# Optimization experiments

Measured on AMD Instinct MI355X. Metric: run time of the kernel, lower is better.

Reference implementation:

```python
import jax, jax.numpy as jnp
import numpy as np

T, S, N, E, H, FF = 1024, 2048, 4, 1024, 16, 4096
HD = E // H
EPS = 1e-5


def layer_norm(x, g, b):
    mu = jnp.mean(x, axis=-1, keepdims=True)
    var = jnp.mean(jnp.square(x - mu), axis=-1, keepdims=True)
    return (x - mu) / jnp.sqrt(var + EPS) * g + b


def mha(q_in, k_in, v_in, w_in, b_in, w_out, b_out):
    # q_in: (T,N,E), k_in/v_in: (S,N,E); matches torch F.linear with (3E,E) weight
    t, n, e = q_in.shape
    s = k_in.shape[0]
    wq, wk, wv = jnp.split(w_in, 3, axis=0)
    bq, bk, bv = jnp.split(b_in, 3)
    q = (q_in @ wq.T + bq) * (HD ** -0.5)
    k = k_in @ wk.T + bk
    v = v_in @ wv.T + bv
    # (L,N,E) -> (N*H, L, HD)
    q = q.reshape(t, n * H, HD).transpose(1, 0, 2)
    k = k.reshape(s, n * H, HD).transpose(1, 0, 2)
    v = v.reshape(s, n * H, HD).transpose(1, 0, 2)
    attn = jax.nn.softmax(jnp.einsum('bth,bsh->bts', q, k), axis=-1)
    out = jnp.einsum('bts,bsh->bth', attn, v)  # (N*H, T, HD)
    out = out.transpose(1, 0, 2).reshape(t, n, e)
    return out @ w_out.T + b_out


def setup_inputs() -> dict:
    key = jax.random.key(0)
    ks = jax.random.split(key, 16)
    p = lambda k, shape: jax.random.normal(k, shape, dtype=jnp.float32) * 0.02
    return {
        'tgt': jax.random.normal(ks[0], (T, N, E), dtype=jnp.float32),
        'memory': jax.random.normal(ks[1], (S, N, E), dtype=jnp.float32),
        'sa_w_in': p(ks[2], (3 * E, E)), 'sa_b_in': jnp.zeros((3 * E,), jnp.float32),
        'sa_w_out': p(ks[3], (E, E)), 'sa_b_out': jnp.zeros((E,), jnp.float32),
        'ca_w_in': p(ks[4], (3 * E, E)), 'ca_b_in': jnp.zeros((3 * E,), jnp.float32),
        'ca_w_out': p(ks[5], (E, E)), 'ca_b_out': jnp.zeros((E,), jnp.float32),
        'w1': p(ks[6], (FF, E)), 'b1': jnp.zeros((FF,), jnp.float32),
        'w2': p(ks[7], (E, FF)), 'b2': jnp.zeros((E,), jnp.float32),
        'ln1_g': jnp.ones((E,), jnp.float32), 'ln1_b': jnp.zeros((E,), jnp.float32),
        'ln2_g': jnp.ones((E,), jnp.float32), 'ln2_b': jnp.zeros((E,), jnp.float32),
        'ln3_g': jnp.ones((E,), jnp.float32), 'ln3_b': jnp.zeros((E,), jnp.float32),
    }


def reference(tgt, memory, sa_w_in, sa_b_in, sa_w_out, sa_b_out,
              ca_w_in, ca_b_in, ca_w_out, ca_b_out,
              w1, b1, w2, b2, ln1_g, ln1_b, ln2_g, ln2_b, ln3_g, ln3_b):
    # self-attention block (post-LN residual); dropout = identity (eval mode)
    tgt2 = mha(tgt, tgt, tgt, sa_w_in, sa_b_in, sa_w_out, sa_b_out)
    x = layer_norm(tgt + tgt2, ln1_g, ln1_b)
    # cross-attention block
    tgt2 = mha(x, memory, memory, ca_w_in, ca_b_in, ca_w_out, ca_b_out)
    x = layer_norm(x + tgt2, ln2_g, ln2_b)
    # FFN with relu
    tgt2 = jax.nn.relu(x @ w1.T + b1) @ w2.T + b2
    return layer_norm(x + tgt2, ln3_g, ln3_b)
```

## Files before the change

### kernel.cpp

```cpp
#include <hip/hip_runtime.h>


typedef __bf16 bf16x8 __attribute__((ext_vector_type(8)));
typedef float  f32x4  __attribute__((ext_vector_type(4)));
typedef float  f32x16 __attribute__((ext_vector_type(16)));

#define T_  1024
#define S_  2048
#define NB_ 4
#define E_  1024
#define H_  16
#define HD_ 64
#define FF_ 4096
#define M1_ (T_*NB_)
#define M2_ (S_*NB_)
#define LOG2E 1.44269504088896f

__device__ __forceinline__ unsigned short f2bf(float f){
  unsigned int u = __builtin_bit_cast(unsigned int, f);
  u += 0x7fffu + ((u>>16)&1u);
  return (unsigned short)(u>>16);
}
__device__ __forceinline__ float bf2f(unsigned short h){
  unsigned int u = ((unsigned int)h)<<16;
  return __builtin_bit_cast(float, u);
}

__device__ __forceinline__ void gload16(unsigned short* l, const unsigned short* g){
  __builtin_amdgcn_global_load_lds(
      (const __attribute__((address_space(1))) unsigned int*)g,
      (__attribute__((address_space(3))) unsigned int*)l, 16, 0, 0);
}

__device__ __forceinline__ void perm32swap(unsigned &a, unsigned &b){
  asm("v_permlane32_swap_b32 %0, %1" : "+v"(a), "+v"(b));
}

__device__ __forceinline__ int loff(int row, int kc){
  return ((row>>1)<<6) + (((((row&1)<<2)|kc) ^ ((row>>1)&7))<<3);
}

struct CvtSeg { const float* s; unsigned short* d; int n4; };
struct CvtArgs { CvtSeg seg[8]; int blk_end[8]; };
__global__ __launch_bounds__(256) void f2b_multi_k(CvtArgs a){
  const int b = blockIdx.x;
  int si = 0;
  #pragma unroll
  for (int i=0;i<8;i++) if (b >= a.blk_end[i]) si = i+1;
  const int base = si ? a.blk_end[si-1] : 0;
  const int i4 = (b - base)*256 + threadIdx.x;
  if (i4 >= a.seg[si].n4) return;
  float4 f = ((const float4*)a.seg[si].s)[i4];
  union { unsigned short u[4]; uint2 v; } t;
  t.u[0]=f2bf(f.x); t.u[1]=f2bf(f.y); t.u[2]=f2bf(f.z); t.u[3]=f2bf(f.w);
  ((uint2*)a.seg[si].d)[i4] = t.v;
}

template<int FLAGS>
__global__ __launch_bounds__(512, 2) void gemm8_k(
    const unsigned short* __restrict__ A, int lda,
    const unsigned short* __restrict__ B, int ldb,
    const float* __restrict__ bias,
    unsigned short* __restrict__ Cb,
    int M, int N, int K)
{
  __shared__ unsigned short a_sh[4][256*32];
  __shared__ unsigned short b_sh[4][256*32];
  const int tid  = threadIdx.x;
  const int wave = tid>>6, lane = tid&63;
  const int l15 = lane&15, l4 = lane>>4;

  int bid = blockIdx.x;
  if ((gridDim.x & 7) == 0){ const int cpx = gridDim.x>>3; bid = (bid&7)*cpx + (bid>>3); }
  const int nbm = M>>8;
  const int bm = bid % nbm, bn = bid / nbm;
  const int brow = bm<<8, bcol = bn<<8;
  const int wm0 = (wave>>2)*128, wn = (wave&3)*64;
  const int NT = K>>5;

  int ldsl[2]; const unsigned short* pA[2]; const unsigned short* pB[2];
  #pragma unroll
  for (int i=0;i<2;i++){
    const int l = i*512 + wave*64 + lane;
    const int grp = l>>3, sl = (l&7) ^ (grp&7);
    const int row = (grp<<1)|(sl>>2), c = sl&3;
    ldsl[i] = l<<3;
    pA[i] = A + (size_t)(brow + row)*lda + (c<<3);
    pB[i] = B + (size_t)(bcol + row)*ldb + (c<<3);
  }

  f32x4 acc[8][4] = {};

  auto stageA = [&](int t){
    unsigned short* s = a_sh[t&3];
    #pragma unroll
    for (int i=0;i<2;i++) gload16(&s[ldsl[i]], pA[i] + t*32);
  };
  auto stageB = [&](int t){
    unsigned short* s = b_sh[t&3];
    #pragma unroll
    for (int i=0;i<2;i++) gload16(&s[ldsl[i]], pB[i] + t*32);
  };

  stageA(0); stageB(0); stageA(1); stageB(1);
  asm volatile("s_waitcnt vmcnt(4)" ::: "memory");
  __builtin_amdgcn_s_barrier();

  for (int t=0; t<NT; ++t){
    const unsigned short* as = a_sh[t&3];
    const unsigned short* bs = b_sh[t&3];
    const bool pre = (t+2 < NT);

    if (pre) stageA(t+2);
    bf16x8 bf[4], af[4];
    #pragma unroll
    for (int n=0;n<4;n++) bf[n] = *(const bf16x8*)&bs[loff(wn + n*16 + l15, l4)];
    #pragma unroll
    for (int m=0;m<4;m++) af[m] = *(const bf16x8*)&as[loff(wm0 + m*16 + l15, l4)];
    __builtin_amdgcn_s_setprio(1);
    #pragma unroll
    for (int m=0;m<4;m++)
      #pragma unroll
      for (int n=0;n<4;n++)
        acc[m][n] = __builtin_amdgcn_mfma_f32_16x16x32_bf16(af[m], bf[n], acc[m][n], 0,0,0);
    __builtin_amdgcn_s_setprio(0);
    __builtin_amdgcn_s_barrier();

    if (pre) stageB(t+2);
    #pragma unroll
    for (int m=0;m<4;m++) af[m] = *(const bf16x8*)&as[loff(wm0 + 64 + m*16 + l15, l4)];
    __builtin_amdgcn_s_setprio(1);
    #pragma unroll
    for (int m=0;m<4;m++)
      #pragma unroll
      for (int n=0;n<4;n++)
        acc[4+m][n] = __builtin_amdgcn_mfma_f32_16x16x32_bf16(af[m], bf[n], acc[4+m][n], 0,0,0);
    __builtin_amdgcn_s_setprio(0);
    if (pre) asm volatile("s_waitcnt vmcnt(4)" ::: "memory");
    else     asm volatile("s_waitcnt vmcnt(0)" ::: "memory");
    __builtin_amdgcn_s_barrier();
  }

  #pragma unroll
  for (int mi=0;mi<8;mi++){
    #pragma unroll
    for (int r=0;r<4;r++){
      const int rr = brow + wm0 + mi*16 + l4*4 + r;
      #pragma unroll
      for (int n=0;n<4;n++){
        const int cc = bcol + wn + n*16 + l15;
        float v = acc[mi][n][r] + bias[cc];
        if (FLAGS & 1) v = fmaxf(v, 0.f);
        Cb[(size_t)rr*N + cc] = f2bf(v);
      }
    }
  }
}

template<int FLAGS, int BN>
__global__ __launch_bounds__(256) void gemm_k(
    const unsigned short* __restrict__ A, int lda,
    const unsigned short* __restrict__ B, int ldb,
    const float* __restrict__ bias,
    const float* __restrict__ res,
    unsigned short* __restrict__ Cb, float* __restrict__ Cf,
    int M, int N, int K)
{
  constexpr int NW = BN/32;
  __shared__ unsigned short a_sh[128*64];
  __shared__ unsigned short b_sh[BN*64];
  const int tid  = threadIdx.x;
  const int wave = tid>>6;
  const int lane = tid&63;
  const int l15 = lane&15, l4 = lane>>4;
  const int row0 = blockIdx.x*128, col0 = blockIdx.y*BN;
  const int wm = (wave>>1)*64, wn = (wave&1)*(BN/2);

  const int lrow = tid>>3;
  const int scol = ((tid&7) ^ (lrow&7)) << 3;
  const int dst8 = (tid&7) << 3;

  f32x4 acc[4][NW] = {};

  for (int k0=0; k0<K; k0+=64){
    const unsigned short* ga = A + (size_t)(row0+lrow)*lda + k0 + scol;
    const unsigned short* gb = B + (size_t)(col0+lrow)*ldb + k0 + scol;
    #pragma unroll
    for (int i=0;i<4;i++)
      gload16(&a_sh[(lrow + i*32)*64 + dst8], ga + (size_t)(i*32)*lda);
    #pragma unroll
    for (int i=0;i<BN/32;i++)
      gload16(&b_sh[(lrow + i*32)*64 + dst8], gb + (size_t)(i*32)*ldb);
    __syncthreads();
    #pragma unroll
    for (int kk=0;kk<2;kk++){
      const int sw = (((kk<<2)|l4) ^ (l15&7)) << 3;
      bf16x8 af[4], bfr[NW];
      #pragma unroll
      for (int m=0;m<4;m++)  af[m]  = *(const bf16x8*)&a_sh[(wm + m*16 + l15)*64 + sw];
      #pragma unroll
      for (int n=0;n<NW;n++) bfr[n] = *(const bf16x8*)&b_sh[(wn + n*16 + l15)*64 + sw];
      #pragma unroll
      for (int m=0;m<4;m++)
        #pragma unroll
        for (int n=0;n<NW;n++)
          acc[m][n] = __builtin_amdgcn_mfma_f32_16x16x32_bf16(af[m], bfr[n], acc[m][n], 0,0,0);
    }
    __syncthreads();
  }

  #pragma unroll
  for (int m=0;m<4;m++){
    #pragma unroll
    for (int r=0;r<4;r++){
      const int rr = row0 + wm + m*16 + l4*4 + r;
      #pragma unroll
      for (int n=0;n<NW;n++){
        const int cc = col0 + wn + n*16 + l15;
        float v = acc[m][n][r] + bias[cc];
        if (FLAGS & 1) v = fmaxf(v, 0.f);
        if (FLAGS & 2) v += res[(size_t)rr*N + cc];
        if (FLAGS & 4) Cb[(size_t)rr*N + cc] = f2bf(v);
        if (FLAGS & 8) Cf[(size_t)rr*N + cc] = v;
      }
    }
  }
}

template<int BN>
__global__ __launch_bounds__(256) void gemm_splitk_k(
    const unsigned short* __restrict__ A, int lda,
    const unsigned short* __restrict__ B, int ldb,
    const float* __restrict__ bias,
    const float* __restrict__ res,
    float* __restrict__ P0, float* __restrict__ P1,
    int M, int N, int K)
{
  constexpr int NW = BN/32;
  __shared__ unsigned short a_sh[128*64];
  __shared__ unsigned short b_sh[BN*64];
  const int tid  = threadIdx.x;
  const int wave = tid>>6;
  const int lane = tid&63;
  const int l15 = lane&15, l4 = lane>>4;
  const int row0 = blockIdx.x*128, col0 = blockIdx.y*BN;
  const int wm = (wave>>1)*64, wn = (wave&1)*(BN/2);
  const int z = blockIdx.z;
  const int kh = K>>1;
  const int kbeg = z*kh;

  const int lrow = tid>>3;
  const int scol = ((tid&7) ^ (lrow&7)) << 3;
  const int dst8 = (tid&7) << 3;

  f32x4 acc[4][NW] = {};

  for (int k0=kbeg; k0<kbeg+kh; k0+=64){
    const unsigned short* ga = A + (size_t)(row0+lrow)*lda + k0 + scol;
    const unsigned short* gb = B + (size_t)(col0+lrow)*ldb + k0 + scol;
    #pragma unroll
    for (int i=0;i<4;i++)
      gload16(&a_sh[(lrow + i*32)*64 + dst8], ga + (size_t)(i*32)*lda);
    #pragma unroll
    for (int i=0;i<BN/32;i++)
      gload16(&b_sh[(lrow + i*32)*64 + dst8], gb + (size_t)(i*32)*ldb);
    __syncthreads();
    #pragma unroll
    for (int kk=0;kk<2;kk++){
      const int sw = (((kk<<2)|l4) ^ (l15&7)) << 3;
      bf16x8 af[4], bfr[NW];
      #pragma unroll
      for (int m=0;m<4;m++)  af[m]  = *(const bf16x8*)&a_sh[(wm + m*16 + l15)*64 + sw];
      #pragma unroll
      for (int n=0;n<NW;n++) bfr[n] = *(const bf16x8*)&b_sh[(wn + n*16 + l15)*64 + sw];
      #pragma unroll
      for (int m=0;m<4;m++)
        #pragma unroll
        for (int n=0;n<NW;n++)
          acc[m][n] = __builtin_amdgcn_mfma_f32_16x16x32_bf16(af[m], bfr[n], acc[m][n], 0,0,0);
    }
    __syncthreads();
  }

  float* out = z ? P1 : P0;
  #pragma unroll
  for (int m=0;m<4;m++){
    #pragma unroll
    for (int r=0;r<4;r++){
      const int rr = row0 + wm + m*16 + l4*4 + r;
      #pragma unroll
      for (int n=0;n<NW;n++){
        const int cc = col0 + wn + n*16 + l15;
        float v = acc[m][n][r];
        if (!z) v += bias[cc] + res[(size_t)rr*N + cc];
        out[(size_t)rr*N + cc] = v;
      }
    }
  }
}

template<int BN>
__global__ __launch_bounds__(256) void gemm_scat_k(
    const unsigned short* __restrict__ A, int lda,
    const unsigned short* __restrict__ B, int ldb,
    const float* __restrict__ bias,
    unsigned short* __restrict__ qb, unsigned short* __restrict__ kb,
    unsigned short* __restrict__ vtb,
    int M, int N, int K, int nq, int nk, int Lq, int Lkv, float qscale)
{
  constexpr int NW = BN/32;
  constexpr int SMEM_ELEMS = (BN==128) ? (128*132) : (128*64 + BN*64);
  __shared__ unsigned short smem[SMEM_ELEMS];
  unsigned short* a_sh = smem;
  unsigned short* b_sh = smem + 128*64;
  const int tid  = threadIdx.x;
  const int wave = tid>>6, lane = tid&63;
  const int l15 = lane&15, l4 = lane>>4;
  const int row0 = blockIdx.x*128, col0 = blockIdx.y*BN;
  const int wm = (wave>>1)*64, wn = (wave&1)*(BN/2);

  const int lrow = tid>>3;
  const int scol = ((tid&7) ^ (lrow&7)) << 3;
  const int dst8 = (tid&7) << 3;

  f32x4 acc[4][NW] = {};

  for (int k0=0; k0<K; k0+=64){
    const unsigned short* ga = A + (size_t)(row0+lrow)*lda + k0 + scol;
    const unsigned short* gb = B + (size_t)(col0+lrow)*ldb + k0 + scol;
    #pragma unroll
    for (int i=0;i<4;i++)
      gload16(&a_sh[(lrow + i*32)*64 + dst8], ga + (size_t)(i*32)*lda);
    #pragma unroll
    for (int i=0;i<BN/32;i++)
      gload16(&b_sh[(lrow + i*32)*64 + dst8], gb + (size_t)(i*32)*ldb);
    __syncthreads();
    #pragma unroll
    for (int kk=0;kk<2;kk++){
      const int sw = (((kk<<2)|l4) ^ (l15&7)) << 3;
      bf16x8 af[4], bfr[NW];
      #pragma unroll
      for (int m=0;m<4;m++)  af[m]  = *(const bf16x8*)&a_sh[(wm + m*16 + l15)*64 + sw];
      #pragma unroll
      for (int n=0;n<NW;n++) bfr[n] = *(const bf16x8*)&b_sh[(wn + n*16 + l15)*64 + sw];
      #pragma unroll
      for (int m=0;m<4;m++)
        #pragma unroll
        for (int n=0;n<NW;n++)
          acc[m][n] = __builtin_amdgcn_mfma_f32_16x16x32_bf16(af[m], bfr[n], acc[m][n], 0,0,0);
    }
    __syncthreads();
  }

  if (col0 < nq + nk){
    const bool isq = (col0 < nq);
    unsigned short* dst = isq ? qb : kb;
    const int  base  = isq ? 0 : nq;
    const int  L     = isq ? Lq : Lkv;
    const float scale = isq ? qscale : 1.0f;
    #pragma unroll
    for (int m=0;m<4;m++){
      #pragma unroll
      for (int r=0;r<4;r++){
        const int rr = row0 + wm + m*16 + l4*4 + r;
        const int t = rr>>2, nn = rr&3;
        #pragma unroll
        for (int n=0;n<NW;n++){
          const int cc = col0 + wn + n*16 + l15;
          const int e = cc - base, h = e>>6, d = e&63;
          const float v = (acc[m][n][r] + bias[cc]) * scale;
          dst[((size_t)(nn*H_ + h)*L + t)*HD_ + d] = f2bf(v);
        }
      }
    }
  } else if constexpr (BN == 128){
    unsigned short* cT = smem;
    #pragma unroll
    for (int m=0;m<4;m++){
      const int tl = ((wm + m*16)>>2) + l4;
      #pragma unroll
      for (int n=0;n<4;n++){
        const int ccl = wn + n*16 + l15;
        const float bi = bias[col0 + ccl];
        #pragma unroll
        for (int r=0;r<4;r++)
          cT[ccl*132 + r*32 + tl] = f2bf(acc[m][n][r] + bi);
      }
    }
    __syncthreads();
    const int t0 = row0>>2;
    const int tl4 = tid&7, c5 = tid>>3;
    const int voff = nq + nk;
    #pragma unroll
    for (int i=0;i<16;i++){
      const int combo = i*32 + c5;
      const int nn = combo&3, ccl = combo>>2;
      const int e = col0 + ccl - voff, h = e>>6, d = e&63;
      const uint2 val = *(const uint2*)&cT[ccl*132 + nn*32 + tl4*4];
      *(uint2*)(vtb + (size_t)((nn*H_ + h)*HD_ + d)*Lkv + t0 + tl4*4) = val;
    }
  }
}

template<bool PARTIAL, int NT>
__global__ __launch_bounds__(256,3) void attn_k(
    const unsigned short* __restrict__ qb, const unsigned short* __restrict__ kb,
    const unsigned short* __restrict__ vtb,
    unsigned short* __restrict__ o_out, float* __restrict__ l_out,
    int T, int S)
{
  static_assert((NT & 1) == 0 && NT >= 4, "NT even");
  __shared__ unsigned short k_sh[2][64*64];
  __shared__ unsigned short v_sh[2][64*64];
  __shared__ float bc_sh[4][32];
  const int tid  = threadIdx.x;
  const int wave = tid>>6, lane = tid&63;
  const int l31  = lane&31;
  const int hv   = lane>>5;
  const int bh   = blockIdx.x;
  const int z    = blockIdx.z;
  const int s_begin = z * (NT*64);
  const int q0   = blockIdx.y*128 + wave*32;
  const size_t qbase = (size_t)bh*T*HD_;
  const size_t kbase = (size_t)bh*S*HD_;
  const size_t vbase = (size_t)bh*HD_*S;

  const int strow = tid>>3;
  const int stch  = tid&7;
  const int sc_sw = (stch ^ (strow&7)) << 3;
  const int dst8  = stch<<3;
  const unsigned short* gk0 = kb  + kbase + (size_t)s_begin*HD_;
  const unsigned short* gv0 = vtb + vbase + s_begin;

  auto stageK = [&](int t, int slot){
    const unsigned short* g = gk0 + (size_t)(t*64)*HD_;
    gload16(&k_sh[slot][(strow   )*64 + dst8], g + (size_t)(strow   )*HD_ + sc_sw);
    gload16(&k_sh[slot][(strow+32)*64 + dst8], g + (size_t)(strow+32)*HD_ + sc_sw);
  };
  auto stageV = [&](int t, int slot){
    const unsigned short* g = gv0 + t*64;
    gload16(&v_sh[slot][(strow   )*64 + dst8], g + (size_t)(strow   )*S + sc_sw);
    gload16(&v_sh[slot][(strow+32)*64 + dst8], g + (size_t)(strow+32)*S + sc_sw);
  };

  bf16x8 qf[4];
  #pragma unroll
  for (int p=0;p<4;p++)
    qf[p] = *(const bf16x8*)(qb + qbase + (size_t)(q0 + l31)*HD_ + p*16 + hv*8);
  asm volatile("" ::: "memory");

  stageK(0, 0);

  f32x16 o0 = {}, o1 = {};
  float rsa = 0.f, rsb = 0.f;
  bf16x8 paA[4], paB[4];

  auto QK = [&](const unsigned short* ksh, f32x16& s0, f32x16& s1){
    #pragma unroll
    for (int p=0;p<4;p++){
      const int slot = 2*p + hv;
      bf16x8 kf0 = *(const bf16x8*)&ksh[(l31     )*64 + ((slot ^ (l31&7))<<3)];
      bf16x8 kf1 = *(const bf16x8*)&ksh[(l31 + 32)*64 + ((slot ^ (l31&7))<<3)];
      s0 = __builtin_amdgcn_mfma_f32_32x32x16_bf16(kf0, qf[p], s0, 0,0,0);
      s1 = __builtin_amdgcn_mfma_f32_32x32x16_bf16(kf1, qf[p], s1, 0,0,0);
    }
  };
  auto PV = [&](const unsigned short* vsh, const bf16x8* pa){
    #pragma unroll
    for (int ks=0;ks<4;ks++){
      const int slot = 2*ks + hv;
      bf16x8 vf0 = *(const bf16x8*)&vsh[(l31     )*64 + ((slot ^ (l31&7))<<3)];
      bf16x8 vf1 = *(const bf16x8*)&vsh[(l31 + 32)*64 + ((slot ^ (l31&7))<<3)];
      o0 = __builtin_amdgcn_mfma_f32_32x32x16_bf16(pa[ks], vf0, o0, 0,0,0);
      o1 = __builtin_amdgcn_mfma_f32_32x32x16_bf16(pa[ks], vf1, o1, 0,0,0);
    }
  };
  auto SM = [&](f32x16& s0, f32x16& s1, bf16x8* pa){
    #pragma unroll
    for (int r=0;r<16;r++){
      s0[r] = __builtin_amdgcn_exp2f(s0[r]);
      s1[r] = __builtin_amdgcn_exp2f(s1[r]);
    }
    #pragma unroll
    for (int r=0;r<16;r+=2){
      rsa += s0[r]   + s1[r];
      rsb += s0[r+1] + s1[r+1];
    }
    #pragma unroll
    for (int ks=0;ks<4;ks++){
      const int base = 8*(ks&1);
      unsigned pkA0, pkA1, pkB0, pkB1;
      if (ks < 2){
        asm("v_cvt_pk_bf16_f32 %0, %1, %2" : "=v"(pkA0) : "v"(s0[base+0]), "v"(s0[base+1]));
        asm("v_cvt_pk_bf16_f32 %0, %1, %2" : "=v"(pkA1) : "v"(s0[base+2]), "v"(s0[base+3]));
        asm("v_cvt_pk_bf16_f32 %0, %1, %2" : "=v"(pkB0) : "v"(s0[base+4]), "v"(s0[base+5]));
        asm("v_cvt_pk_bf16_f32 %0, %1, %2" : "=v"(pkB1) : "v"(s0[base+6]), "v"(s0[base+7]));
      } else {
        asm("v_cvt_pk_bf16_f32 %0, %1, %2" : "=v"(pkA0) : "v"(s1[base+0]), "v"(s1[base+1]));
        asm("v_cvt_pk_bf16_f32 %0, %1, %2" : "=v"(pkA1) : "v"(s1[base+2]), "v"(s1[base+3]));
        asm("v_cvt_pk_bf16_f32 %0, %1, %2" : "=v"(pkB0) : "v"(s1[base+4]), "v"(s1[base+5]));
        asm("v_cvt_pk_bf16_f32 %0, %1, %2" : "=v"(pkB1) : "v"(s1[base+6]), "v"(s1[base+7]));
      }
      perm32swap(pkA0, pkB0);
      perm32swap(pkA1, pkB1);
      union { unsigned w[4]; bf16x8 v; } u;
      u.w[0] = pkA0; u.w[1] = pkA1; u.w[2] = pkB0; u.w[3] = pkB1;
      pa[ks] = u.v;
    }
  };

  {
    stageK(1, 1);
    stageV(0, 0);
    asm volatile("s_waitcnt vmcnt(4)" ::: "memory");
    __builtin_amdgcn_s_barrier();
    f32x16 s0 = {}, s1 = {};
    __builtin_amdgcn_s_setprio(1);
    QK(k_sh[0], s0, s1);
    __builtin_amdgcn_s_setprio(0);
    SM(s0, s1, paA);
    __builtin_amdgcn_s_barrier();
  }

  auto BODY = [&](int i, const bf16x8* paPrev, bf16x8* paCur){
    const int kt = (i+1 < NT) ? (i+1) : (NT-1);
    stageK(kt, (i+1)&1);
    stageV(i, i&1);
    asm volatile("s_waitcnt vmcnt(4)" ::: "memory");
    __builtin_amdgcn_s_barrier();
    f32x16 s0 = {}, s1 = {};
    __builtin_amdgcn_s_setprio(1);
    QK(k_sh[i&1], s0, s1);
    PV(v_sh[(i+1)&1], paPrev);
    __builtin_amdgcn_s_setprio(0);
    SM(s0, s1, paCur);
    __builtin_amdgcn_s_barrier();
  };

  for (int ii=1; ii+1<NT; ii+=2){
    BODY(ii,   paA, paB);
    BODY(ii+1, paB, paA);
  }
  BODY(NT-1, paA, paB);

  asm volatile("s_waitcnt vmcnt(0)" ::: "memory");
  __builtin_amdgcn_s_barrier();
  __builtin_amdgcn_s_setprio(1);
  PV(v_sh[(NT-1)&1], paB);
  __builtin_amdgcn_s_setprio(0);

  float l_run = rsa + rsb;
  {
    unsigned a_ = __builtin_bit_cast(unsigned, l_run), b_ = a_;
    perm32swap(a_, b_);
    l_run += __builtin_bit_cast(float, hv ? a_ : b_);
  }

  if constexpr (PARTIAL){
    const size_t obase = (size_t)(z*64 + bh)*T;
    #pragma unroll
    for (int r=0;r<16;r++){
      const int qr = (r&3) + 8*(r>>2) + 4*hv;
      unsigned short* op = o_out + (obase + q0 + qr)*HD_;
      op[l31]      = f2bf(o0[r]);
      op[l31 + 32] = f2bf(o1[r]);
    }
    if (hv == 0) l_out[obase + q0 + l31] = l_run;
  } else {
    bc_sh[wave][l31] = 1.f / l_run;
    const int nb = bh>>4, hh = bh&15;
    #pragma unroll
    for (int r=0;r<16;r++){
      const int qr  = (r&3) + 8*(r>>2) + 4*hv;
      const float inv = bc_sh[wave][qr];
      const int t = q0 + qr;
      unsigned short* op = o_out + ((size_t)t*NB_ + nb)*E_ + hh*HD_;
      op[l31]      = f2bf(o0[r]*inv);
      op[l31 + 32] = f2bf(o1[r]*inv);
    }
  }
}

__global__ __launch_bounds__(256) void comb_k(
    const unsigned short* __restrict__ opart, const float* __restrict__ lpart,
    unsigned short* __restrict__ outb, int T)
{
  const int bh = blockIdx.y;
  const int t  = blockIdx.x*4 + (threadIdx.x>>6);
  const int d  = threadIdx.x&63;
  const size_t half = (size_t)64*T;
  const size_t row  = (size_t)bh*T + t;
  const float o = bf2f(opart[row*HD_ + d]) + bf2f(opart[(half + row)*HD_ + d]);
  const float l = lpart[row] + lpart[half + row];
  const int nb = bh>>4, hh = bh&15;
  outb[((size_t)t*NB_ + nb)*E_ + hh*HD_ + d] = f2bf(o / l);
}

__global__ __launch_bounds__(256) void ln_k(
    const float* __restrict__ p0, const float* __restrict__ p1,
    const float* __restrict__ g, const float* __restrict__ bb,
    float* __restrict__ of, unsigned short* __restrict__ ob)
{
  const int row = blockIdx.x, tid = threadIdx.x;
  const size_t base = (size_t)row*E_;
  float v[4];
  #pragma unroll
  for (int i=0;i<4;i++){
    const int col = tid + 256*i;
    v[i] = p0[base + col] + p1[base + col];
  }
  float s  = v[0]+v[1]+v[2]+v[3];
  float s2 = v[0]*v[0]+v[1]*v[1]+v[2]*v[2]+v[3]*v[3];
  #pragma unroll
  for (int off=32; off>0; off>>=1){
    s  += __shfl_down(s, off);
    s2 += __shfl_down(s2, off);
  }
  __shared__ float red[8];
  if ((tid&63)==0){ red[tid>>6] = s; red[4+(tid>>6)] = s2; }
  __syncthreads();
  s  = red[0]+red[1]+red[2]+red[3];
  s2 = red[4]+red[5]+red[6]+red[7];
  const float mu   = s * (1.f/E_);
  const float var  = s2 * (1.f/E_) - mu*mu;
  const float rstd = rsqrtf(var + 1e-5f);
  #pragma unroll
  for (int i=0;i<4;i++){
    const int col = tid + 256*i;
    const float y = (v[i]-mu)*rstd*g[col] + bb[col];
    if (of) of[base + col] = y;
    if (ob) ob[base + col] = f2bf(y);
  }
}

extern "C" void kernel_launch(void* const* d_in, const int* in_sizes, int n_in,
                              void* d_out, int out_size, void* d_ws, size_t ws_size,
                              hipStream_t stream)
{
  const float* tgt      = (const float*)d_in[0];
  const float* mem      = (const float*)d_in[1];
  const float* sa_w_in  = (const float*)d_in[2];
  const float* sa_b_in  = (const float*)d_in[3];
  const float* sa_w_out = (const float*)d_in[4];
  const float* sa_b_out = (const float*)d_in[5];
  const float* ca_w_in  = (const float*)d_in[6];
  const float* ca_b_in  = (const float*)d_in[7];
  const float* ca_w_out = (const float*)d_in[8];
  const float* ca_b_out = (const float*)d_in[9];
  const float* w1 = (const float*)d_in[10];
  const float* b1 = (const float*)d_in[11];
  const float* w2 = (const float*)d_in[12];
  const float* b2 = (const float*)d_in[13];
  const float* ln1_g=(const float*)d_in[14]; const float* ln1_b=(const float*)d_in[15];
  const float* ln2_g=(const float*)d_in[16]; const float* ln2_b=(const float*)d_in[17];
  const float* ln3_g=(const float*)d_in[18]; const float* ln3_b=(const float*)d_in[19];

  char* ws = (char*)d_ws;
  size_t off = 0;
  auto alloc = [&](size_t bytes)->char* {
    char* p = ws + off; off += (bytes + 255) & ~(size_t)255; return p;
  };
  unsigned short* w_sa_in_b  = (unsigned short*)alloc((size_t)3*E_*E_*2);
  unsigned short* w_sa_out_b = (unsigned short*)alloc((size_t)E_*E_*2);
  unsigned short* w_ca_in_b  = (unsigned short*)alloc((size_t)3*E_*E_*2);
  unsigned short* w_ca_out_b = (unsigned short*)alloc((size_t)E_*E_*2);
  unsigned short* w1_b  = (unsigned short*)alloc((size_t)FF_*E_*2);
  unsigned short* w2_b  = (unsigned short*)alloc((size_t)E_*FF_*2);
  unsigned short* tgt_b = (unsigned short*)alloc((size_t)M1_*E_*2);
  unsigned short* mem_b = (unsigned short*)alloc((size_t)M2_*E_*2);
  unsigned short* qbuf  = (unsigned short*)alloc((size_t)64*T_*HD_*2);
  unsigned short* kbuf  = (unsigned short*)alloc((size_t)64*S_*HD_*2);
  unsigned short* vtbuf = (unsigned short*)alloc((size_t)64*S_*HD_*2);
  unsigned short* cbuf  = (unsigned short*)alloc((size_t)M1_*FF_*2);
  unsigned short* atto  = (unsigned short*)alloc((size_t)M1_*E_*2);
  unsigned short* opart = (unsigned short*)alloc((size_t)2*64*T_*HD_*2);
  float*          lpart = (float*)alloc((size_t)2*64*T_*4);
  float* resf = (float*)alloc((size_t)M1_*E_*4);
  float* xf   = (float*)alloc((size_t)M1_*E_*4);
  unsigned short* xb = (unsigned short*)alloc((size_t)M1_*E_*2);
  (void)ws_size; (void)in_sizes; (void)n_in; (void)out_size;

  float* P1 = (float*)opart;

  const float QSCALE = 0.125f * LOG2E;

  {
    CvtArgs a;
    const float* srcs[8] = {tgt, mem, sa_w_in, sa_w_out, ca_w_in, ca_w_out, w1, w2};
    unsigned short* dsts[8] = {tgt_b, mem_b, w_sa_in_b, w_sa_out_b, w_ca_in_b, w_ca_out_b, w1_b, w2_b};
    size_t ns[8] = {(size_t)M1_*E_, (size_t)M2_*E_, (size_t)3*E_*E_, (size_t)E_*E_,
                    (size_t)3*E_*E_, (size_t)E_*E_, (size_t)FF_*E_, (size_t)E_*FF_};
    int blk = 0;
    for (int i=0;i<8;i++){
      a.seg[i].s = srcs[i]; a.seg[i].d = dsts[i]; a.seg[i].n4 = (int)(ns[i]/4);
      blk += (a.seg[i].n4 + 255)/256;
      a.blk_end[i] = blk;
    }
    f2b_multi_k<<<blk, 256, 0, stream>>>(a);
  }

  gemm_scat_k<128><<<dim3(M1_/128, (3*E_)/128), 256, 0, stream>>>(
      tgt_b, E_, w_sa_in_b, E_, sa_b_in, qbuf, kbuf, vtbuf,
      M1_, 3*E_, E_, E_, E_, T_, T_, QSCALE);
  attn_k<false,16><<<dim3(64, T_/128, 1), 256, 0, stream>>>(
      qbuf, kbuf, vtbuf, atto, nullptr, T_, T_);
  gemm_splitk_k<64><<<dim3(M1_/128, E_/64, 2), 256, 0, stream>>>(
      atto, E_, w_sa_out_b, E_, sa_b_out, tgt, resf, P1, M1_, E_, E_);
  ln_k<<<M1_, 256, 0, stream>>>(resf, P1, ln1_g, ln1_b, xf, xb);

  gemm_scat_k<128><<<dim3(M2_/128, (2*E_)/128), 256, 0, stream>>>(
      mem_b, E_, w_ca_in_b + (size_t)E_*E_, E_, ca_b_in + E_, nullptr, kbuf, vtbuf,
      M2_, 2*E_, E_, 0, E_, T_, S_, QSCALE);
  gemm_scat_k<64><<<dim3(M1_/128, E_/64), 256, 0, stream>>>(
      xb, E_, w_ca_in_b, E_, ca_b_in, qbuf, nullptr, nullptr,
      M1_, E_, E_, E_, 0, T_, S_, QSCALE);
  attn_k<true,16><<<dim3(64, T_/128, 2), 256, 0, stream>>>(
      qbuf, kbuf, vtbuf, opart, lpart, T_, S_);
  comb_k<<<dim3(T_/4, 64), 256, 0, stream>>>(opart, lpart, atto, T_);
  gemm_splitk_k<64><<<dim3(M1_/128, E_/64, 2), 256, 0, stream>>>(
      atto, E_, w_ca_out_b, E_, ca_b_out, xf, resf, P1, M1_, E_, E_);
  ln_k<<<M1_, 256, 0, stream>>>(resf, P1, ln2_g, ln2_b, xf, xb);

  gemm8_k<5><<<(M1_/256)*(FF_/256), 512, 0, stream>>>(
      xb, E_, w1_b, E_, b1, cbuf, M1_, FF_, E_);
  gemm_splitk_k<64><<<dim3(M1_/128, E_/64, 2), 256, 0, stream>>>(
      cbuf, FF_, w2_b, FF_, b2, xf, resf, P1, M1_, E_, FF_);
  ln_k<<<M1_, 256, 0, stream>>>(resf, P1, ln3_g, ln3_b, (float*)d_out, nullptr);
}
```

Measured before the change: 389.1 us.

## Use 256x256 gemm8 kernel with scatter epilogue for cross-attention K/V projection

Replaces the 128-tile scatter GEMM for the memory K/V projection with the larger 256x256 gemm8 kernel. It adds an epilogue that writes K in head-major layout and writes V transposed through an LDS staging buffer so the global stores are coalesced. The gemm8 mainloop also deepens prefetch from 2 to 3 stages, with extra barriers so the 4-slot ring buffer is not overwritten while still being read. The extra barriers may add sync overhead in the FFN GEMM, which uses the same kernel.

```diff
diff --git a/kernel.cpp b/kernel.cpp
--- a/kernel.cpp
+++ b/kernel.cpp
@@ -56,16 +56,16 @@
   ((uint2*)a.seg[si].d)[i4] = t.v;
 }
 
-template<int FLAGS>
+template<int FLAGS, int EPI>
 __global__ __launch_bounds__(512, 2) void gemm8_k(
     const unsigned short* __restrict__ A, int lda,
     const unsigned short* __restrict__ B, int ldb,
     const float* __restrict__ bias,
     unsigned short* __restrict__ Cb,
-    int M, int N, int K)
+    unsigned short* __restrict__ kb, unsigned short* __restrict__ vtb,
+    int M, int N, int K, int Lkv, int nk)
 {
-  __shared__ unsigned short a_sh[4][256*32];
-  __shared__ unsigned short b_sh[4][256*32];
+  __shared__ unsigned short smem[2][4][256*32];
   const int tid  = threadIdx.x;
   const int wave = tid>>6, lane = tid&63;
   const int l15 = lane&15, l4 = lane>>4;
@@ -92,31 +92,32 @@
   f32x4 acc[8][4] = {};
 
   auto stageA = [&](int t){
-    unsigned short* s = a_sh[t&3];
+    unsigned short* s = smem[0][t&3];
     #pragma unroll
     for (int i=0;i<2;i++) gload16(&s[ldsl[i]], pA[i] + t*32);
   };
   auto stageB = [&](int t){
-    unsigned short* s = b_sh[t&3];
+    unsigned short* s = smem[1][t&3];
     #pragma unroll
     for (int i=0;i<2;i++) gload16(&s[ldsl[i]], pB[i] + t*32);
   };
 
-  stageA(0); stageB(0); stageA(1); stageB(1);
-  asm volatile("s_waitcnt vmcnt(4)" ::: "memory");
+  stageA(0); stageB(0); stageA(1); stageB(1); stageA(2); stageB(2);
+  asm volatile("s_waitcnt vmcnt(8)" ::: "memory");
   __builtin_amdgcn_s_barrier();
 
   for (int t=0; t<NT; ++t){
-    const unsigned short* as = a_sh[t&3];
-    const unsigned short* bs = b_sh[t&3];
-    const bool pre = (t+2 < NT);
-
-    if (pre) stageA(t+2);
+    const unsigned short* as = smem[0][t&3];
+    const unsigned short* bs = smem[1][t&3];
+    const bool pre = (t+3 < NT);
+
+    if (pre) stageA(t+3);
     bf16x8 bf[4], af[4];
     #pragma unroll
     for (int n=0;n<4;n++) bf[n] = *(const bf16x8*)&bs[loff(wn + n*16 + l15, l4)];
     #pragma unroll
     for (int m=0;m<4;m++) af[m] = *(const bf16x8*)&as[loff(wm0 + m*16 + l15, l4)];
+    __builtin_amdgcn_s_barrier();
     __builtin_amdgcn_s_setprio(1);
     #pragma unroll
     for (int m=0;m<4;m++)
@@ -126,9 +127,10 @@
     __builtin_amdgcn_s_setprio(0);
     __builtin_amdgcn_s_barrier();
 
-    if (pre) stageB(t+2);
+    if (pre) stageB(t+3);
     #pragma unroll
     for (int m=0;m<4;m++) af[m] = *(const bf16x8*)&as[loff(wm0 + 64 + m*16 + l15, l4)];
+    __builtin_amdgcn_s_barrier();
     __builtin_amdgcn_s_setprio(1);
     #pragma unroll
     for (int m=0;m<4;m++)
@@ -136,22 +138,69 @@
       for (int n=0;n<4;n++)
         acc[4+m][n] = __builtin_amdgcn_mfma_f32_16x16x32_bf16(af[m], bf[n], acc[4+m][n], 0,0,0);
     __builtin_amdgcn_s_setprio(0);
-    if (pre) asm volatile("s_waitcnt vmcnt(4)" ::: "memory");
-    else     asm volatile("s_waitcnt vmcnt(0)" ::: "memory");
+    if (pre)            asm volatile("s_waitcnt vmcnt(8)" ::: "memory");
+    else if (t+2 < NT)  asm volatile("s_waitcnt vmcnt(4)" ::: "memory");
+    else                asm volatile("s_waitcnt vmcnt(0)" ::: "memory");
     __builtin_amdgcn_s_barrier();
   }
 
-  #pragma unroll
-  for (int mi=0;mi<8;mi++){
-    #pragma unroll
-    for (int r=0;r<4;r++){
-      const int rr = brow + wm0 + mi*16 + l4*4 + r;
-      #pragma unroll
-      for (int n=0;n<4;n++){
-        const int cc = bcol + wn + n*16 + l15;
-        float v = acc[mi][n][r] + bias[cc];
-        if (FLAGS & 1) v = fmaxf(v, 0.f);
-        Cb[(size_t)rr*N + cc] = f2bf(v);
+  if constexpr (EPI == 0){
+    #pragma unroll
+    for (int mi=0;mi<8;mi++){
+      #pragma unroll
+      for (int r=0;r<4;r++){
+        const int rr = brow + wm0 + mi*16 + l4*4 + r;
+        #pragma unroll
+        for (int n=0;n<4;n++){
+          const int cc = bcol + wn + n*16 + l15;
+          float v = acc[mi][n][r] + bias[cc];
+          if (FLAGS & 1) v = fmaxf(v, 0.f);
+          Cb[(size_t)rr*N + cc] = f2bf(v);
+        }
+      }
+    }
+  } else {
+    if (bcol < nk){
+      #pragma unroll
+      for (int mi=0;mi<8;mi++){
+        #pragma unroll
+        for (int r=0;r<4;r++){
+          const int rr = brow + wm0 + mi*16 + l4*4 + r;
+          const int t = rr>>2, nn = rr&3;
+          #pragma unroll
+          for (int n=0;n<4;n++){
+            const int cc = bcol + wn + n*16 + l15;
+            const int h = cc>>6, d = cc&63;
+            kb[((size_t)(nn*H_ + h)*Lkv + t)*HD_ + d] = f2bf(acc[mi][n][r] + bias[cc]);
+          }
+        }
+      }
+    } else {
+      unsigned short* cT = &smem[0][0][0];
+      #pragma unroll
+      for (int mi=0;mi<8;mi++){
+        const int tl = (wm0>>2) + mi*4 + l4;
+        #pragma unroll
+        for (int n=0;n<4;n++){
+          const int ccl = wn + n*16 + l15;
+          const float bi = bias[bcol + ccl];
+          #pragma unroll
+          for (int r=0;r<4;r++){
+            const int unit = r*8 + (tl>>3);
+            cT[ccl*256 + ((unit ^ (ccl&7))<<3) + (tl&7)] = f2bf(acc[mi][n][r] + bi);
+          }
+        }
+      }
+      __syncthreads();
+      const int t0 = brow>>2;
+      #pragma unroll
+      for (int i=0;i<16;i++){
+        const int ch = i*512 + tid;
+        const int tl8 = ch&7, nn = (ch>>3)&3, ccl = ch>>5;
+        const int e = bcol - nk + ccl, h = e>>6, d = e&63;
+        const int unit = (nn<<3) | tl8;
+        const uint2 v = *(const uint2*)&cT[ccl*256 + ((unit ^ (ccl&7))<<3)];
+        *(uint2*)(vtb + ((size_t)(nn*H_ + h)*HD_ + d)*Lkv + t0 + tl8*8) = v;
       }
     }
   }
@@ -708,9 +757,9 @@
       atto, E_, w_sa_out_b, E_, sa_b_out, tgt, resf, P1, M1_, E_, E_);
   ln_k<<<M1_, 256, 0, stream>>>(resf, P1, ln1_g, ln1_b, xf, xb);
 
-  gemm_scat_k<128><<<dim3(M2_/128, (2*E_)/128), 256, 0, stream>>>(
-      mem_b, E_, w_ca_in_b + (size_t)E_*E_, E_, ca_b_in + E_, nullptr, kbuf, vtbuf,
-      M2_, 2*E_, E_, 0, E_, T_, S_, QSCALE);
+  gemm8_k<0,1><<<(M2_/256)*((2*E_)/256), 512, 0, stream>>>(
+      mem_b, E_, w_ca_in_b + (size_t)E_*E_, E_, ca_b_in + E_, nullptr,
+      kbuf, vtbuf, M2_, 2*E_, E_, S_, E_);
   gemm_scat_k<64><<<dim3(M1_/128, E_/64), 256, 0, stream>>>(
       xb, E_, w_ca_in_b, E_, ca_b_in, qbuf, nullptr, nullptr,
       M1_, E_, E_, E_, 0, T_, S_, QSCALE);
@@ -721,8 +770,8 @@
       atto, E_, w_ca_out_b, E_, ca_b_out, xf, resf, P1, M1_, E_, E_);
   ln_k<<<M1_, 256, 0, stream>>>(resf, P1, ln2_g, ln2_b, xf, xb);
 
-  gemm8_k<5><<<(M1_/256)*(FF_/256), 512, 0, stream>>>(
-      xb, E_, w1_b, E_, b1, cbuf, M1_, FF_, E_);
+  gemm8_k<5,0><<<(M1_/256)*(FF_/256), 512, 0, stream>>>(
+      xb, E_, w1_b, E_, b1, cbuf, nullptr, nullptr, M1_, FF_, E_, 0, 0);
   gemm_splitk_k<64><<<dim3(M1_/128, E_/64, 2), 256, 0, stream>>>(
       cbuf, FF_, w2_b, FF_, b2, xf, resf, P1, M1_, E_, FF_);
   ln_k<<<M1_, 256, 0, stream>>>(resf, P1, ln3_g, ln3_b, (float*)d_out, nullptr);
```

Result: faster. 378.8 us (-2.7%).
